# Kernel tuning notes

Hardware: AMD Instinct MI355X
Metric: run time of the kernel (lower is better)

## Reference

```python
import jax, jax.numpy as jnp
import numpy as np

NUM_HEADS = 8
NUM_GROUPS = 32
EPS = 1e-5
RESCALE = 1.0


def setup_inputs() -> dict:
    key = jax.random.key(0)
    ks = jax.random.split(key, 7)
    b, c, h, w = 16, 512, 32, 32
    return {
        "x": jax.random.normal(ks[0], (b, c, h, w), jnp.float32),
        "norm_w": jax.random.normal(ks[1], (c,), jnp.float32),
        "norm_b": jax.random.normal(ks[2], (c,), jnp.float32),
        "qkv_w": jax.random.normal(ks[3], (3 * c, c), jnp.float32) * (c ** -0.5),
        "qkv_b": jax.random.normal(ks[4], (3 * c,), jnp.float32) * 0.02,
        "proj_w": jax.random.normal(ks[5], (c, c), jnp.float32) * (c ** -0.5),
        "proj_b": jax.random.normal(ks[6], (c,), jnp.float32) * 0.02,
    }


def _group_norm(x, w, b):
    # x: [B, C, L]
    B, C, L = x.shape
    g = x.reshape(B, NUM_GROUPS, (C // NUM_GROUPS) * L)
    mu = jnp.mean(g, axis=-1, keepdims=True)
    var = jnp.var(g, axis=-1, keepdims=True)
    g = (g - mu) * jax.lax.rsqrt(var + EPS)
    return g.reshape(B, C, L) * w[None, :, None] + b[None, :, None]


def reference(x, norm_w, norm_b, qkv_w, qkv_b, proj_w, proj_b):
    b, c, hh, ww = x.shape
    L = hh * ww
    H = NUM_HEADS
    ch = c // H  # head dim

    xr = x.reshape(b, c, L)
    hid = _group_norm(xr, norm_w, norm_b)

    # 1x1 conv1d == matmul over channel dim: [3c, c] @ [b, c, L]
    qkv = jnp.einsum('oc,bcl->bol', qkv_w, hid) + qkv_b[None, :, None]
    # torch: reshape(b*H, 3*ch, L).split(ch) -> per-head contiguous [q|k|v] blocks
    qkv = qkv.reshape(b, H, 3, ch, L)
    q, k, v = qkv[:, :, 0], qkv[:, :, 1], qkv[:, :, 2]  # [b, H, ch, L]

    scale = 1.0 / (ch ** 0.25)
    weight = jnp.einsum('bhct,bhcs->bhts', q * scale, k * scale)
    weight = jax.nn.softmax(weight.astype(jnp.float32), axis=-1).astype(weight.dtype)
    a = jnp.einsum('bhts,bhcs->bhct', weight, v)  # [b, H, ch, L]

    h = a.reshape(b, c, L)
    h = jnp.einsum('oc,bcl->bol', proj_w, h) + proj_b[None, :, None]
    h = h.reshape(b, c, hh, ww)
    return (x + h) / RESCALE
```

## Files before the change

kernel.cpp:

```cpp
#include <hip/hip_runtime.h>
#include <hip/hip_bf16.h>
#include <stdint.h>


using f32x4  = __attribute__((ext_vector_type(4))) float;
using bf16x8 = __attribute__((ext_vector_type(8))) __bf16;
using s8v    = __attribute__((ext_vector_type(8))) short;
using s4v    = __attribute__((ext_vector_type(4))) short;

__device__ __forceinline__ short f2bf(float f){
  union { float f; unsigned u; } c; c.f = f;
  unsigned r = (c.u + 0x7FFFu + ((c.u >> 16) & 1u)) >> 16;
  return (short)r;
}

__device__ __forceinline__ void gl_lds16(const void* g, void* l){
  __builtin_amdgcn_global_load_lds((const __attribute__((address_space(1))) void*)g,
                                   (__attribute__((address_space(3))) void*)l, 16, 0, 0);
}

__global__ void k_convw(const float* __restrict__ qw, const float* __restrict__ pw,
                        short* __restrict__ qwb, short* __restrict__ pwb){
  int i = blockIdx.x * 256 + threadIdx.x;
  if (i < 1536*512) qwb[i] = f2bf(qw[i]);
  else              pwb[i - 1536*512] = f2bf(pw[i - 1536*512]);
}

__global__ __launch_bounds__(256) void k_gnorm(const float* __restrict__ x,
                                               const float* __restrict__ w,
                                               const float* __restrict__ bia,
                                               short* __restrict__ hid){
  int b = blockIdx.x >> 5;
  int g = blockIdx.x & 31;
  int tid = threadIdx.x;
  const float* xg = x + ((size_t)b*512 + g*16)*1024;
  int l0 = tid * 4;
  float v[16][4];
  float s1 = 0.f, s2 = 0.f;
  #pragma unroll
  for (int c = 0; c < 16; c++){
    f32x4 t = *(const f32x4*)(xg + c*1024 + l0);
    #pragma unroll
    for (int j = 0; j < 4; j++){ v[c][j] = t[j]; s1 += t[j]; s2 += t[j]*t[j]; }
  }
  #pragma unroll
  for (int m = 32; m; m >>= 1){ s1 += __shfl_xor(s1, m); s2 += __shfl_xor(s2, m); }
  __shared__ float r1[4], r2[4];
  int wv = tid >> 6, ln = tid & 63;
  if (ln == 0){ r1[wv] = s1; r2[wv] = s2; }
  __syncthreads();
  s1 = r1[0]+r1[1]+r1[2]+r1[3];
  s2 = r2[0]+r2[1]+r2[2]+r2[3];
  float mu = s1 * (1.f/16384.f);
  float var = s2 * (1.f/16384.f) - mu*mu;
  float rs = rsqrtf(var + 1e-5f);
  float ww[16], bb[16];
  #pragma unroll
  for (int c = 0; c < 16; c++){ ww[c] = w[g*16+c]*rs; bb[c] = bia[g*16+c]; }
  #pragma unroll
  for (int j = 0; j < 4; j++){
    short o[16];
    #pragma unroll
    for (int c = 0; c < 16; c++) o[c] = f2bf((v[c][j]-mu)*ww[c] + bb[c]);
    short* dst = hid + ((size_t)(b*1024 + l0 + j))*512 + g*16;
    *(s8v*)dst     = *(s8v*)o;
    *(s8v*)(dst+8) = *(s8v*)(o+8);
  }
}

template<int EPI>
__global__ __launch_bounds__(256) void k_gemm(
    const short* __restrict__ A, const short* __restrict__ Bm,
    const float* __restrict__ bias, const float* __restrict__ xres,
    short* __restrict__ q_t, short* __restrict__ k_t, short* __restrict__ v_t,
    float* __restrict__ outp)
{
  __shared__ short Al[2][128*64];
  __shared__ short Bl[2][128*64];
  int id = blockIdx.x;
  int xcd = id & 7, ix = id >> 3;
  int n0 = (xcd + 8*(ix & 15)) * 128;
  int m0 = (ix >> 4) * 128;
  int tid = threadIdx.x;
  int lane = tid & 63;
  int wv = tid >> 6;
  int wr = wv >> 1, wc = wv & 1;
  f32x4 acc[4][4] = {};

  auto STAGE = [&](int db, int k0){
    #pragma unroll
    for (int i = 0; i < 8; i++){
      int cc = wv*8 + i;
      if (cc < 16){
        int slot = cc*64 + lane;
        int row = slot >> 3, off = slot & 7;
        gl_lds16(A + (size_t)(m0+row)*512 + k0 + (off ^ (row&7))*8,
                 (char*)Al[db] + cc*1024);
      } else {
        int slot = (cc-16)*64 + lane;
        int row = slot >> 3, off = slot & 7;
        gl_lds16(Bm + (size_t)(n0+row)*512 + k0 + (off ^ (row&7))*8,
                 (char*)Bl[db] + (cc-16)*1024);
      }
    }
  };

  STAGE(0, 0);
  for (int t = 0; t < 8; t++){
    STAGE((t+1)&1, ((t+1)&7)*64);
    asm volatile("s_waitcnt vmcnt(8)" ::: "memory");
    __builtin_amdgcn_s_barrier();
    int db = t & 1;
    #pragma unroll
    for (int kk = 0; kk < 2; kk++){
      bf16x8 af[4], bf[4];
      #pragma unroll
      for (int m = 0; m < 4; m++){
        int row = wr*64 + m*16 + (lane&15);
        int byte = row*128 + (((kk*64) + ((lane>>4)*16)) ^ ((row&7)<<4));
        af[m] = *(const bf16x8*)((char*)Al[db] + byte);
      }
      #pragma unroll
      for (int n = 0; n < 4; n++){
        int row = wc*64 + n*16 + (lane&15);
        int byte = row*128 + (((kk*64) + ((lane>>4)*16)) ^ ((row&7)<<4));
        bf[n] = *(const bf16x8*)((char*)Bl[db] + byte);
      }
      __builtin_amdgcn_s_setprio(1);
      #pragma unroll
      for (int m = 0; m < 4; m++)
        #pragma unroll
        for (int n = 0; n < 4; n++)
          acc[m][n] = __builtin_amdgcn_mfma_f32_16x16x32_bf16(af[m], bf[n], acc[m][n], 0, 0, 0);
      __builtin_amdgcn_s_setprio(0);
    }
    __builtin_amdgcn_s_barrier();
  }

  if (EPI == 0){
    #pragma unroll
    for (int m = 0; m < 4; m++){
      int ob  = m0 + wr*64 + m*16 + ((lane>>4)<<2);
      int hh  = ob / 192;
      int rem = ob % 192;
      int sel = rem >> 6;
      int c0  = rem & 63;
      float bs[4];
      #pragma unroll
      for (int r = 0; r < 4; r++) bs[r] = bias[ob+r];
      #pragma unroll
      for (int n = 0; n < 4; n++){
        int nn = n0 + wc*64 + n*16 + (lane&15);
        int bb = nn >> 10, ll = nn & 1023;
        int bh = bb*8 + hh;
        if (sel == 2){
          short* dst = v_t + ((size_t)bh*64 + c0)*1024 + ll;
          #pragma unroll
          for (int r = 0; r < 4; r++) dst[r*1024] = f2bf(acc[m][n][r] + bs[r]);
        } else {
          float sc = (sel == 0) ? 0.125f : 1.0f;
          short o4[4];
          #pragma unroll
          for (int r = 0; r < 4; r++) o4[r] = f2bf((acc[m][n][r] + bs[r]) * sc);
          short* dst = (sel == 0 ? q_t : k_t) + ((size_t)bh*1024 + ll)*64 + c0;
          *(s4v*)dst = *(s4v*)o4;
        }
      }
    }
  } else {
    #pragma unroll
    for (int m = 0; m < 4; m++){
      int ob = m0 + wr*64 + m*16 + ((lane>>4)<<2);
      float bs[4];
      #pragma unroll
      for (int r = 0; r < 4; r++) bs[r] = bias[ob+r];
      #pragma unroll
      for (int n = 0; n < 4; n++){
        int nn = n0 + wc*64 + n*16 + (lane&15);
        int bb = nn >> 10, ll = nn & 1023;
        #pragma unroll
        for (int r = 0; r < 4; r++){
          size_t idx = ((size_t)bb*512 + ob + r)*1024 + ll;
          outp[idx] = xres[idx] + acc[m][n][r] + bs[r];
        }
      }
    }
  }
}

__global__ __launch_bounds__(256, 4) void k_attn(
    const short* __restrict__ q_t, const short* __restrict__ k_t,
    const short* __restrict__ v_t, short* __restrict__ a_bt)
{
  __shared__ short Kl[2][64*64];
  __shared__ short Vl[2][64*64];
  int id = blockIdx.x;
  int xcd = id & 7, ix = id >> 3;
  int bh = xcd*16 + (ix >> 3);
  int qb = ix & 7;
  int bb = bh >> 3, hh = bh & 7;
  int tid = threadIdx.x;
  int lane = tid & 63;
  int wv = tid >> 6;
  int l15 = lane & 15, g = lane >> 4;

  bf16x8 qf[2][2];
  #pragma unroll
  for (int qt = 0; qt < 2; qt++){
    const short* qbase = q_t + ((size_t)bh*1024 + qb*128 + qt*64 + wv*16 + l15)*64 + g*8;
    qf[qt][0] = *(const bf16x8*)(qbase);
    qf[qt][1] = *(const bf16x8*)(qbase + 32);
  }
  asm volatile("" :: "v"(qf[0][0]), "v"(qf[0][1]), "v"(qf[1][0]), "v"(qf[1][1]));

  auto STAGE = [&](int db, int s0){
    #pragma unroll
    for (int i = 0; i < 4; i++){
      int cc = wv*4 + i;
      if (cc < 8){
        int slot = cc*64 + lane;
        int row = slot >> 3, off = slot & 7;
        gl_lds16(k_t + ((size_t)bh*1024 + s0 + row)*64 + (off ^ (row&7))*8,
                 (char*)Kl[db] + cc*1024);
      } else {
        int lam = (cc-8)*1024 + lane*16;
        int sblk = lam >> 11;
        int d    = (lam >> 5) & 63;
        int inn  = (lam & 31) >> 1;
        gl_lds16(v_t + ((size_t)bh*64 + d)*1024 + s0 + sblk*16 + inn,
                 (char*)Vl[db] + (cc-8)*1024);
      }
    }
  };

  f32x4 o[2][4] = {};
  float psum[2] = {0.f, 0.f};

  STAGE(0, 0);
  for (int t = 0; t < 16; t++){
    STAGE((t+1)&1, ((t+1)&15)*64);
    asm volatile("s_waitcnt vmcnt(4)" ::: "memory");
    __builtin_amdgcn_s_barrier();
    int db = t & 1;

    f32x4 sc[2][4] = {};
    #pragma unroll
    for (int j = 0; j < 4; j++){
      #pragma unroll
      for (int ks = 0; ks < 2; ks++){
        int row = j*16 + l15;
        int byte = row*128 + (((ks*64) + (g*16)) ^ ((row&7)<<4));
        bf16x8 kf = *(const bf16x8*)((char*)Kl[db] + byte);
        __builtin_amdgcn_s_setprio(1);
        #pragma unroll
        for (int qt = 0; qt < 2; qt++)
          sc[qt][j] = __builtin_amdgcn_mfma_f32_16x16x32_bf16(kf, qf[qt][ks], sc[qt][j], 0, 0, 0);
        __builtin_amdgcn_s_setprio(0);
      }
    }

    #pragma unroll
    for (int ks = 0; ks < 2; ks++){
      bf16x8 pa[2];
      #pragma unroll
      for (int qt = 0; qt < 2; qt++){
        #pragma unroll
        for (int i2 = 0; i2 < 8; i2++){
          float e = __expf(sc[qt][2*ks + (i2>>2)][i2&3]);
          psum[qt] += e;
          pa[qt][i2] = (__bf16)e;
        }
      }
      #pragma unroll
      for (int jd = 0; jd < 4; jd++){
        int d = jd*16 + l15;
        union { s4v h[2]; bf16x8 b; } vb;
        vb.h[0] = *(const s4v*)((char*)Vl[db] + (2*ks+0)*2048 + d*32 + g*8);
        vb.h[1] = *(const s4v*)((char*)Vl[db] + (2*ks+1)*2048 + d*32 + g*8);
        __builtin_amdgcn_s_setprio(1);
        #pragma unroll
        for (int qt = 0; qt < 2; qt++)
          o[qt][jd] = __builtin_amdgcn_mfma_f32_16x16x32_bf16(pa[qt], vb.b, o[qt][jd], 0, 0, 0);
        __builtin_amdgcn_s_setprio(0);
      }
    }
    __builtin_amdgcn_s_barrier();
  }

  #pragma unroll
  for (int qt = 0; qt < 2; qt++){
    psum[qt] += __shfl_xor(psum[qt], 16);
    psum[qt] += __shfl_xor(psum[qt], 32);
  }
  #pragma unroll
  for (int qt = 0; qt < 2; qt++){
    #pragma unroll
    for (int r = 0; r < 4; r++){
      float lr = __shfl(psum[qt], g*4 + r);
      float inv = 1.f / lr;
      int qrow = qb*128 + qt*64 + wv*16 + g*4 + r;
      #pragma unroll
      for (int jd = 0; jd < 4; jd++)
        a_bt[((size_t)bb*1024 + qrow)*512 + hh*64 + jd*16 + l15] = f2bf(o[qt][jd][r] * inv);
    }
  }
}

extern "C" void kernel_launch(void* const* d_in, const int* in_sizes, int n_in,
                              void* d_out, int out_size, void* d_ws, size_t ws_size,
                              hipStream_t stream){
  const float* x  = (const float*)d_in[0];
  const float* nw = (const float*)d_in[1];
  const float* nb = (const float*)d_in[2];
  const float* qw = (const float*)d_in[3];
  const float* qb = (const float*)d_in[4];
  const float* pw = (const float*)d_in[5];
  const float* pb = (const float*)d_in[6];
  float* outp = (float*)d_out;

  char* ws = (char*)d_ws;
  short* hid  = (short*)(ws);
  short* qwb  = (short*)(ws + 16777216);
  short* pwb  = (short*)(ws + 18350080);
  short* q_t  = (short*)(ws + 18874368);
  short* k_t  = (short*)(ws + 35651584);
  short* v_t  = (short*)(ws + 52428800);
  short* a_bt = hid;
  if (ws_size < 69206016) return;

  k_convw<<<4096, 256, 0, stream>>>(qw, pw, qwb, pwb);
  k_gnorm<<<512, 256, 0, stream>>>(x, nw, nb, hid);
  k_gemm<0><<<1536, 256, 0, stream>>>(qwb, hid, qb, nullptr, q_t, k_t, v_t, nullptr);
  k_attn<<<1024, 256, 0, stream>>>(q_t, k_t, v_t, a_bt);
  k_gemm<1><<<512, 256, 0, stream>>>(pwb, a_bt, pb, x, nullptr, nullptr, nullptr, outp);
}
```

Measured before the change: 138.1 us.

## Use exp2 with folded log2e scale, MFMA row sums, tiled V layout

The Q scale now includes log2(e), so the softmax exponent becomes a raw hardware exp2 instead of __expf. Row sums come from an MFMA against a ones vector rather than per-lane adds and end-of-kernel shuffles. V is written in a pre-tiled layout so each 64-key block is one contiguous 8KB chunk, which simplifies staging addresses and LDS read indexing. The costs are an extra MFMA per block, row sums computed from bf16-rounded probabilities, and scattered 2-byte stores in the QKV epilogue.

```diff
diff --git a/kernel.cpp b/kernel.cpp
--- a/kernel.cpp
+++ b/kernel.cpp
@@ -12,6 +12,14 @@
   union { float f; unsigned u; } c; c.f = f;
   unsigned r = (c.u + 0x7FFFu + ((c.u >> 16) & 1u)) >> 16;
   return (short)r;
+}
+
+__device__ __forceinline__ float exp2_fast(float x){
+#if __has_builtin(__builtin_amdgcn_exp2f)
+  return __builtin_amdgcn_exp2f(x);
+#else
+  return exp2f(x);
+#endif
 }
 
 __device__ __forceinline__ void gl_lds16(const void* g, void* l){
@@ -154,11 +162,13 @@
         int bb = nn >> 10, ll = nn & 1023;
         int bh = bb*8 + hh;
         if (sel == 2){
-          short* dst = v_t + ((size_t)bh*64 + c0)*1024 + ll;
+          int sl = ll & 63;
+          short* p0 = v_t + ((size_t)bh*16 + (ll>>6))*4096
+                    + (((sl>>4)*4 + ((sl>>2)&3))*4 + (c0>>4))*64 + (c0&15)*4 + (sl&3);
           #pragma unroll
-          for (int r = 0; r < 4; r++) dst[r*1024] = f2bf(acc[m][n][r] + bs[r]);
+          for (int r = 0; r < 4; r++) p0[r*4] = f2bf(acc[m][n][r] + bs[r]);
         } else {
-          float sc = (sel == 0) ? 0.125f : 1.0f;
+          float sc = (sel == 0) ? 0.18033688011112042f : 1.0f;
           short o4[4];
           #pragma unroll
           for (int r = 0; r < 4; r++) o4[r] = f2bf((acc[m][n][r] + bs[r]) * sc);
@@ -213,6 +223,10 @@
   }
   asm volatile("" :: "v"(qf[0][0]), "v"(qf[0][1]), "v"(qf[1][0]), "v"(qf[1][1]));
 
+  bf16x8 onesb;
+  #pragma unroll
+  for (int i = 0; i < 8; i++) onesb[i] = (__bf16)1.0f;
+
   auto STAGE = [&](int db, int s0){
     #pragma unroll
     for (int i = 0; i < 4; i++){
@@ -223,18 +237,14 @@
         gl_lds16(k_t + ((size_t)bh*1024 + s0 + row)*64 + (off ^ (row&7))*8,
                  (char*)Kl[db] + cc*1024);
       } else {
-        int lam = (cc-8)*1024 + lane*16;
-        int sblk = lam >> 11;
-        int d    = (lam >> 5) & 63;
-        int inn  = (lam & 31) >> 1;
-        gl_lds16(v_t + ((size_t)bh*64 + d)*1024 + s0 + sblk*16 + inn,
+        gl_lds16(v_t + ((size_t)bh*16 + (s0>>6))*4096 + (cc-8)*512 + lane*8,
                  (char*)Vl[db] + (cc-8)*1024);
       }
     }
   };
 
   f32x4 o[2][4] = {};
-  float psum[2] = {0.f, 0.f};
+  f32x4 osum[2] = {};
 
   STAGE(0, 0);
   for (int t = 0; t < 16; t++){
@@ -265,18 +275,15 @@
       #pragma unroll
       for (int qt = 0; qt < 2; qt++){
         #pragma unroll
-        for (int i2 = 0; i2 < 8; i2++){
-          float e = __expf(sc[qt][2*ks + (i2>>2)][i2&3]);
-          psum[qt] += e;
-          pa[qt][i2] = (__bf16)e;
-        }
+        for (int i2 = 0; i2 < 8; i2++)
+          pa[qt][i2] = (__bf16)exp2_fast(sc[qt][2*ks + (i2>>2)][i2&3]);
+        osum[qt] = __builtin_amdgcn_mfma_f32_16x16x32_bf16(pa[qt], onesb, osum[qt], 0, 0, 0);
       }
       #pragma unroll
       for (int jd = 0; jd < 4; jd++){
-        int d = jd*16 + l15;
         union { s4v h[2]; bf16x8 b; } vb;
-        vb.h[0] = *(const s4v*)((char*)Vl[db] + (2*ks+0)*2048 + d*32 + g*8);
-        vb.h[1] = *(const s4v*)((char*)Vl[db] + (2*ks+1)*2048 + d*32 + g*8);
+        vb.h[0] = *(const s4v*)((char*)Vl[db] + ks*4096        + g*512 + jd*128 + l15*8);
+        vb.h[1] = *(const s4v*)((char*)Vl[db] + ks*4096 + 2048 + g*512 + jd*128 + l15*8);
         __builtin_amdgcn_s_setprio(1);
         #pragma unroll
         for (int qt = 0; qt < 2; qt++)
@@ -289,15 +296,9 @@
 
   #pragma unroll
   for (int qt = 0; qt < 2; qt++){
-    psum[qt] += __shfl_xor(psum[qt], 16);
-    psum[qt] += __shfl_xor(psum[qt], 32);
-  }
-  #pragma unroll
-  for (int qt = 0; qt < 2; qt++){
     #pragma unroll
     for (int r = 0; r < 4; r++){
-      float lr = __shfl(psum[qt], g*4 + r);
-      float inv = 1.f / lr;
+      float inv = 1.f / osum[qt][r];
       int qrow = qb*128 + qt*64 + wv*16 + g*4 + r;
       #pragma unroll
       for (int jd = 0; jd < 4; jd++)
```

Result: faster. 131.1 us (-5.1%).
